# Kernel tuning notes

Measured on AMD Instinct MI355X. Metric: run time of the kernel, lower is better.

The kernel has to match this reference:

```python
import jax, jax.numpy as jnp
import numpy as np

N_NODES = 50000
N_EDGES = 800000
IN_FEATS = 96
HIDDEN = 48


def setup_inputs() -> dict:
    key = jax.random.key(0)
    ks = jax.random.split(key, 16)
    x = jax.random.normal(ks[0], (N_NODES, IN_FEATS), dtype=jnp.float32)
    edge_index = jax.random.randint(ks[1], (2, N_EDGES), 0, N_NODES, dtype=jnp.int32)

    def lin(k, fan_in, fan_out):
        s = 1.0 / np.sqrt(fan_in)
        return jax.random.uniform(k, (fan_in, fan_out), jnp.float32, -s, s)

    return {
        "x": x,
        "edge_index": edge_index,
        # SAGEConv layer 0: in -> hidden
        "w_self0": lin(ks[2], IN_FEATS, HIDDEN),
        "w_neigh0": lin(ks[3], IN_FEATS, HIDDEN),
        "b0": jnp.zeros((HIDDEN,), jnp.float32),
        # SAGEConv layer 1: hidden -> hidden
        "w_self1": lin(ks[4], HIDDEN, HIDDEN),
        "w_neigh1": lin(ks[5], HIDDEN, HIDDEN),
        "b1": jnp.zeros((HIDDEN,), jnp.float32),
        # SAGEConv layer 2: hidden -> hidden
        "w_self2": lin(ks[6], HIDDEN, HIDDEN),
        "w_neigh2": lin(ks[7], HIDDEN, HIDDEN),
        "b2": jnp.zeros((HIDDEN,), jnp.float32),
        # prediction head: hidden -> 1
        "w_pred": lin(ks[8], HIDDEN, 1),
        "b_pred": jnp.zeros((1,), jnp.float32),
    }


def _sage_mean(x, src, dst, deg_inv, w_self, w_neigh, b):
    # mean over in-neighbors: gather src features, segment-sum at dst, / in-degree
    agg = jax.ops.segment_sum(x[src], dst, num_segments=N_NODES) * deg_inv  # [N, F]
    return x @ w_self + agg @ w_neigh + b


def reference(x, edge_index, w_self0, w_neigh0, b0, w_self1, w_neigh1, b1,
              w_self2, w_neigh2, b2, w_pred, b_pred):
    src, dst = edge_index[0], edge_index[1]
    deg = jax.ops.segment_sum(jnp.ones((src.shape[0],), x.dtype), dst,
                              num_segments=N_NODES)
    deg_inv = (1.0 / jnp.maximum(deg, 1.0))[:, None]  # isolated nodes -> 0 agg

    h = jax.nn.relu(_sage_mean(x, src, dst, deg_inv, w_self0, w_neigh0, b0))
    h = jax.nn.relu(_sage_mean(h, src, dst, deg_inv, w_self1, w_neigh1, b1))
    h = jax.nn.relu(_sage_mean(h, src, dst, deg_inv, w_self2, w_neigh2, b2))
    return h @ w_pred + b_pred  # [N, 1]
```

## Files before the change

### kernel.cpp

```cpp
#include <hip/hip_runtime.h>


constexpr int HID = 48;
constexpr int MAXDEG = 64;
constexpr int GNB = 64;

__global__ __launch_bounds__(128) void fill_proj_k(
    const float* __restrict__ X, const float* __restrict__ Wn,
    const float* __restrict__ Ws, const float* __restrict__ bias,
    float* __restrict__ p_out, float* __restrict__ s_out, int n_nodes,
    const int* __restrict__ src, const int* __restrict__ dst,
    int* __restrict__ cnt, unsigned short* __restrict__ buckets,
    int n_edges, int gemm_blocks) {
    __shared__ float wn_lds[96 * HID];
    __shared__ float ws_lds[96 * HID];
    __shared__ float bias_lds[HID];
    const int t = threadIdx.x;

    if ((int)blockIdx.x >= gemm_blocks) {
        int base = (blockIdx.x - gemm_blocks) * 256 + t;
        int e0 = base, e1 = base + 128;
        if (e0 < n_edges) {
            int d = dst[e0];
            int s = src[e0];
            int pos = atomicAdd(&cnt[d], 1);
            if (pos < MAXDEG) buckets[(size_t)d * MAXDEG + pos] = (unsigned short)s;
        }
        if (e1 < n_edges) {
            int d = dst[e1];
            int s = src[e1];
            int pos = atomicAdd(&cnt[d], 1);
            if (pos < MAXDEG) buckets[(size_t)d * MAXDEG + pos] = (unsigned short)s;
        }
        return;
    }

    for (int i = t; i < 96 * HID; i += 128) {
        wn_lds[i] = Wn[i];
        ws_lds[i] = Ws[i];
    }
    if (t < HID) bias_lds[t] = bias[t];
    __syncthreads();

    const int q = t & 3;
    const int m = t >> 2;
    const int jb = q * 12;
    const int n0 = blockIdx.x * GNB + 2 * m;
    const int n1 = n0 + 1;
    const bool v0 = n0 < n_nodes, v1 = n1 < n_nodes;
    const int cn0 = v0 ? n0 : 0, cn1 = v1 ? n1 : 0;

    float pa[12], pb[12], sa[12], sb[12];
#pragma unroll
    for (int j = 0; j < 12; ++j) {
        pa[j] = 0.0f; pb[j] = 0.0f;
        float b = bias_lds[jb + j];
        sa[j] = b; sb[j] = b;
    }

    const float4* xr0 = reinterpret_cast<const float4*>(X + (size_t)cn0 * 96);
    const float4* xr1 = reinterpret_cast<const float4*>(X + (size_t)cn1 * 96);
#pragma unroll 4
    for (int k4 = 0; k4 < 24; ++k4) {
        float4 xa = xr0[k4];
        float4 xb = xr1[k4];
#pragma unroll
        for (int c = 0; c < 4; ++c) {
            float x0 = (c == 0) ? xa.x : (c == 1) ? xa.y : (c == 2) ? xa.z : xa.w;
            float x1 = (c == 0) ? xb.x : (c == 1) ? xb.y : (c == 2) ? xb.z : xb.w;
            const float4* wnr =
                reinterpret_cast<const float4*>(&wn_lds[(k4 * 4 + c) * HID + jb]);
            const float4* wsr =
                reinterpret_cast<const float4*>(&ws_lds[(k4 * 4 + c) * HID + jb]);
#pragma unroll
            for (int j4 = 0; j4 < 3; ++j4) {
                float4 wv = wnr[j4];
                pa[j4 * 4 + 0] = fmaf(x0, wv.x, pa[j4 * 4 + 0]);
                pa[j4 * 4 + 1] = fmaf(x0, wv.y, pa[j4 * 4 + 1]);
                pa[j4 * 4 + 2] = fmaf(x0, wv.z, pa[j4 * 4 + 2]);
                pa[j4 * 4 + 3] = fmaf(x0, wv.w, pa[j4 * 4 + 3]);
                pb[j4 * 4 + 0] = fmaf(x1, wv.x, pb[j4 * 4 + 0]);
                pb[j4 * 4 + 1] = fmaf(x1, wv.y, pb[j4 * 4 + 1]);
                pb[j4 * 4 + 2] = fmaf(x1, wv.z, pb[j4 * 4 + 2]);
                pb[j4 * 4 + 3] = fmaf(x1, wv.w, pb[j4 * 4 + 3]);
                float4 uv = wsr[j4];
                sa[j4 * 4 + 0] = fmaf(x0, uv.x, sa[j4 * 4 + 0]);
                sa[j4 * 4 + 1] = fmaf(x0, uv.y, sa[j4 * 4 + 1]);
                sa[j4 * 4 + 2] = fmaf(x0, uv.z, sa[j4 * 4 + 2]);
                sa[j4 * 4 + 3] = fmaf(x0, uv.w, sa[j4 * 4 + 3]);
                sb[j4 * 4 + 0] = fmaf(x1, uv.x, sb[j4 * 4 + 0]);
                sb[j4 * 4 + 1] = fmaf(x1, uv.y, sb[j4 * 4 + 1]);
                sb[j4 * 4 + 2] = fmaf(x1, uv.z, sb[j4 * 4 + 2]);
                sb[j4 * 4 + 3] = fmaf(x1, uv.w, sb[j4 * 4 + 3]);
            }
        }
    }
    float4* po0 = reinterpret_cast<float4*>(p_out + (size_t)n0 * HID + jb);
    float4* po1 = reinterpret_cast<float4*>(p_out + (size_t)n1 * HID + jb);
    float4* so0 = reinterpret_cast<float4*>(s_out + (size_t)n0 * HID + jb);
    float4* so1 = reinterpret_cast<float4*>(s_out + (size_t)n1 * HID + jb);
#pragma unroll
    for (int j4 = 0; j4 < 3; ++j4) {
        if (v0) {
            po0[j4] = make_float4(pa[j4 * 4 + 0], pa[j4 * 4 + 1], pa[j4 * 4 + 2], pa[j4 * 4 + 3]);
            so0[j4] = make_float4(sa[j4 * 4 + 0], sa[j4 * 4 + 1], sa[j4 * 4 + 2], sa[j4 * 4 + 3]);
        }
        if (v1) {
            po1[j4] = make_float4(pb[j4 * 4 + 0], pb[j4 * 4 + 1], pb[j4 * 4 + 2], pb[j4 * 4 + 3]);
            so1[j4] = make_float4(sb[j4 * 4 + 0], sb[j4 * 4 + 1], sb[j4 * 4 + 2], sb[j4 * 4 + 3]);
        }
    }
}

__device__ __forceinline__ void gather12(const float* __restrict__ p_in,
                                         const unsigned short* __restrict__ bkt,
                                         int deg, int jb, float4 (&g)[3]) {
    float4 ga0 = make_float4(0.f, 0.f, 0.f, 0.f), ga1 = ga0, ga2 = ga0;
    float4 gb0 = ga0, gb1 = ga0, gb2 = ga0;
    int e = 0;
    for (; e + 2 <= deg; e += 2) {
        int s0 = bkt[e], s1 = bkt[e + 1];
        const float4* r0 = reinterpret_cast<const float4*>(p_in + (size_t)s0 * HID + jb);
        const float4* r1 = reinterpret_cast<const float4*>(p_in + (size_t)s1 * HID + jb);
        float4 a0 = r0[0], a1 = r0[1], a2 = r0[2];
        float4 b0 = r1[0], b1 = r1[1], b2 = r1[2];
        ga0.x += a0.x; ga0.y += a0.y; ga0.z += a0.z; ga0.w += a0.w;
        ga1.x += a1.x; ga1.y += a1.y; ga1.z += a1.z; ga1.w += a1.w;
        ga2.x += a2.x; ga2.y += a2.y; ga2.z += a2.z; ga2.w += a2.w;
        gb0.x += b0.x; gb0.y += b0.y; gb0.z += b0.z; gb0.w += b0.w;
        gb1.x += b1.x; gb1.y += b1.y; gb1.z += b1.z; gb1.w += b1.w;
        gb2.x += b2.x; gb2.y += b2.y; gb2.z += b2.z; gb2.w += b2.w;
    }
    if (e < deg) {
        const float4* r0 = reinterpret_cast<const float4*>(p_in + (size_t)bkt[e] * HID + jb);
        float4 a0 = r0[0], a1 = r0[1], a2 = r0[2];
        ga0.x += a0.x; ga0.y += a0.y; ga0.z += a0.z; ga0.w += a0.w;
        ga1.x += a1.x; ga1.y += a1.y; ga1.z += a1.z; ga1.w += a1.w;
        ga2.x += a2.x; ga2.y += a2.y; ga2.z += a2.z; ga2.w += a2.w;
    }
    g[0] = make_float4(ga0.x + gb0.x, ga0.y + gb0.y, ga0.z + gb0.z, ga0.w + gb0.w);
    g[1] = make_float4(ga1.x + gb1.x, ga1.y + gb1.y, ga1.z + gb1.z, ga1.w + gb1.w);
    g[2] = make_float4(ga2.x + gb2.x, ga2.y + gb2.y, ga2.z + gb2.z, ga2.w + gb2.w);
}

template <bool LAST>
__global__ __launch_bounds__(128) void fused_layer_k(
    const float* __restrict__ p_in, const float* __restrict__ s_in,
    const int* __restrict__ cnt, const unsigned short* __restrict__ buckets,
    const float* __restrict__ wn_next, const float* __restrict__ ws_next,
    const float* __restrict__ b_next, const float* __restrict__ w_pred,
    const float* __restrict__ b_pred, float* __restrict__ p_out,
    float* __restrict__ s_out, float* __restrict__ out, int n_nodes) {
    __shared__ float wn_lds[LAST ? 4 : HID * HID];
    __shared__ float ws_lds[LAST ? 4 : HID * HID];
    __shared__ float bn_lds[HID];
    __shared__ float h_tile[LAST ? 4 : GNB * (HID + 1)];
    __shared__ float wpred_lds[HID];

    const int t = threadIdx.x;
    if (!LAST) {
        for (int i = t; i < HID * HID; i += 128) {
            wn_lds[i] = wn_next[i];
            ws_lds[i] = ws_next[i];
        }
        if (t < HID) bn_lds[t] = b_next[t];
    } else {
        if (t < HID) wpred_lds[t] = w_pred[t];
    }
    __syncthreads();

    const int q = t & 3;
    const int m = t >> 2;
    const int jb = q * 12;
    const int n0 = blockIdx.x * GNB + 2 * m;
    const int n1 = n0 + 1;
    const bool v0 = n0 < n_nodes, v1 = n1 < n_nodes;
    const int cn0 = v0 ? n0 : 0, cn1 = v1 ? n1 : 0;

    const int d0 = min(cnt[cn0], MAXDEG);
    const int d1 = min(cnt[cn1], MAXDEG);
    const float di0 = 1.0f / fmaxf((float)d0, 1.0f);
    const float di1 = 1.0f / fmaxf((float)d1, 1.0f);

    float4 g0[3], g1[3];
    gather12(p_in, buckets + (size_t)cn0 * MAXDEG, d0, jb, g0);
    gather12(p_in, buckets + (size_t)cn1 * MAXDEG, d1, jb, g1);

    const float4* sr0 = reinterpret_cast<const float4*>(s_in + (size_t)cn0 * HID + jb);
    const float4* sr1 = reinterpret_cast<const float4*>(s_in + (size_t)cn1 * HID + jb);
    float h0v[12], h1v[12];
#pragma unroll
    for (int j4 = 0; j4 < 3; ++j4) {
        float4 sv0 = sr0[j4];
        float4 sv1 = sr1[j4];
        h0v[j4 * 4 + 0] = fmaxf(fmaf(di0, g0[j4].x, sv0.x), 0.0f);
        h0v[j4 * 4 + 1] = fmaxf(fmaf(di0, g0[j4].y, sv0.y), 0.0f);
        h0v[j4 * 4 + 2] = fmaxf(fmaf(di0, g0[j4].z, sv0.z), 0.0f);
        h0v[j4 * 4 + 3] = fmaxf(fmaf(di0, g0[j4].w, sv0.w), 0.0f);
        h1v[j4 * 4 + 0] = fmaxf(fmaf(di1, g1[j4].x, sv1.x), 0.0f);
        h1v[j4 * 4 + 1] = fmaxf(fmaf(di1, g1[j4].y, sv1.y), 0.0f);
        h1v[j4 * 4 + 2] = fmaxf(fmaf(di1, g1[j4].z, sv1.z), 0.0f);
        h1v[j4 * 4 + 3] = fmaxf(fmaf(di1, g1[j4].w, sv1.w), 0.0f);
    }

    if (LAST) {
        float s0 = 0.0f, s1 = 0.0f;
#pragma unroll
        for (int j = 0; j < 12; ++j) {
            float wp = wpred_lds[jb + j];
            s0 = fmaf(h0v[j], wp, s0);
            s1 = fmaf(h1v[j], wp, s1);
        }
        s0 += __shfl_xor(s0, 1); s0 += __shfl_xor(s0, 2);
        s1 += __shfl_xor(s1, 1); s1 += __shfl_xor(s1, 2);
        if (q == 0) {
            float bp = b_pred[0];
            if (v0) out[n0] = s0 + bp;
            if (v1) out[n1] = s1 + bp;
        }
        return;
    }

    const int ln0 = 2 * m, ln1 = 2 * m + 1;
#pragma unroll
    for (int j = 0; j < 12; ++j) {
        h_tile[ln0 * (HID + 1) + jb + j] = h0v[j];
        h_tile[ln1 * (HID + 1) + jb + j] = h1v[j];
    }
    __syncthreads();

    float pa[12], pb[12], sa[12], sb[12];
#pragma unroll
    for (int j = 0; j < 12; ++j) {
        pa[j] = 0.0f; pb[j] = 0.0f;
        float b = bn_lds[jb + j];
        sa[j] = b; sb[j] = b;
    }
#pragma unroll 4
    for (int k = 0; k < HID; ++k) {
        float ha = h_tile[ln0 * (HID + 1) + k];
        float hb = h_tile[ln1 * (HID + 1) + k];
        const float4* wnr = reinterpret_cast<const float4*>(&wn_lds[k * HID + jb]);
        const float4* wsr = reinterpret_cast<const float4*>(&ws_lds[k * HID + jb]);
#pragma unroll
        for (int j4 = 0; j4 < 3; ++j4) {
            float4 wv = wnr[j4];
            pa[j4 * 4 + 0] = fmaf(ha, wv.x, pa[j4 * 4 + 0]);
            pa[j4 * 4 + 1] = fmaf(ha, wv.y, pa[j4 * 4 + 1]);
            pa[j4 * 4 + 2] = fmaf(ha, wv.z, pa[j4 * 4 + 2]);
            pa[j4 * 4 + 3] = fmaf(ha, wv.w, pa[j4 * 4 + 3]);
            pb[j4 * 4 + 0] = fmaf(hb, wv.x, pb[j4 * 4 + 0]);
            pb[j4 * 4 + 1] = fmaf(hb, wv.y, pb[j4 * 4 + 1]);
            pb[j4 * 4 + 2] = fmaf(hb, wv.z, pb[j4 * 4 + 2]);
            pb[j4 * 4 + 3] = fmaf(hb, wv.w, pb[j4 * 4 + 3]);
            float4 uv = wsr[j4];
            sa[j4 * 4 + 0] = fmaf(ha, uv.x, sa[j4 * 4 + 0]);
            sa[j4 * 4 + 1] = fmaf(ha, uv.y, sa[j4 * 4 + 1]);
            sa[j4 * 4 + 2] = fmaf(ha, uv.z, sa[j4 * 4 + 2]);
            sa[j4 * 4 + 3] = fmaf(ha, uv.w, sa[j4 * 4 + 3]);
            sb[j4 * 4 + 0] = fmaf(hb, uv.x, sb[j4 * 4 + 0]);
            sb[j4 * 4 + 1] = fmaf(hb, uv.y, sb[j4 * 4 + 1]);
            sb[j4 * 4 + 2] = fmaf(hb, uv.z, sb[j4 * 4 + 2]);
            sb[j4 * 4 + 3] = fmaf(hb, uv.w, sb[j4 * 4 + 3]);
        }
    }
    float4* po0 = reinterpret_cast<float4*>(p_out + (size_t)n0 * HID + jb);
    float4* po1 = reinterpret_cast<float4*>(p_out + (size_t)n1 * HID + jb);
    float4* so0 = reinterpret_cast<float4*>(s_out + (size_t)n0 * HID + jb);
    float4* so1 = reinterpret_cast<float4*>(s_out + (size_t)n1 * HID + jb);
#pragma unroll
    for (int j4 = 0; j4 < 3; ++j4) {
        if (v0) {
            po0[j4] = make_float4(pa[j4 * 4 + 0], pa[j4 * 4 + 1], pa[j4 * 4 + 2], pa[j4 * 4 + 3]);
            so0[j4] = make_float4(sa[j4 * 4 + 0], sa[j4 * 4 + 1], sa[j4 * 4 + 2], sa[j4 * 4 + 3]);
        }
        if (v1) {
            po1[j4] = make_float4(pb[j4 * 4 + 0], pb[j4 * 4 + 1], pb[j4 * 4 + 2], pb[j4 * 4 + 3]);
            so1[j4] = make_float4(sb[j4 * 4 + 0], sb[j4 * 4 + 1], sb[j4 * 4 + 2], sb[j4 * 4 + 3]);
        }
    }
}

extern "C" void kernel_launch(void* const* d_in, const int* in_sizes, int n_in,
                              void* d_out, int out_size, void* d_ws, size_t ws_size,
                              hipStream_t stream) {
    const float* x        = (const float*)d_in[0];
    const int*   ei       = (const int*)d_in[1];
    const float* w_self0  = (const float*)d_in[2];
    const float* w_neigh0 = (const float*)d_in[3];
    const float* b0       = (const float*)d_in[4];
    const float* w_self1  = (const float*)d_in[5];
    const float* w_neigh1 = (const float*)d_in[6];
    const float* b1       = (const float*)d_in[7];
    const float* w_self2  = (const float*)d_in[8];
    const float* w_neigh2 = (const float*)d_in[9];
    const float* b2       = (const float*)d_in[10];
    const float* w_pred   = (const float*)d_in[11];
    const float* b_pred   = (const float*)d_in[12];

    const int n_nodes = in_sizes[0] / 96;
    const int n_edges = in_sizes[1] / 2;
    const int* src = ei;
    const int* dst = ei + n_edges;

    char* wsb = (char*)d_ws;
    int* cnt                = (int*)wsb;              wsb += (size_t)n_nodes * 4;
    unsigned short* buckets = (unsigned short*)wsb;   wsb += (size_t)n_nodes * MAXDEG * 2;
    float* pA = (float*)wsb;                          wsb += (size_t)n_nodes * HID * 4;
    float* sA = (float*)wsb;                          wsb += (size_t)n_nodes * HID * 4;
    float* pB = (float*)wsb;                          wsb += (size_t)n_nodes * HID * 4;
    float* sB = (float*)wsb;                          wsb += (size_t)n_nodes * HID * 4;
    float* out = (float*)d_out;

    const int gnb = (n_nodes + GNB - 1) / GNB;
    const int fb = (n_edges + 255) / 256;

    hipMemsetAsync(cnt, 0, (size_t)n_nodes * 4, stream);

    fill_proj_k<<<gnb + fb, 128, 0, stream>>>(x, w_neigh0, w_self0, b0, pA, sA,
                                              n_nodes, src, dst, cnt, buckets,
                                              n_edges, gnb);
    fused_layer_k<false><<<gnb, 128, 0, stream>>>(pA, sA, cnt, buckets,
                                                  w_neigh1, w_self1, b1,
                                                  nullptr, nullptr, pB, sB,
                                                  nullptr, n_nodes);
    fused_layer_k<false><<<gnb, 128, 0, stream>>>(pB, sB, cnt, buckets,
                                                  w_neigh2, w_self2, b2,
                                                  nullptr, nullptr, pA, sA,
                                                  nullptr, n_nodes);
    fused_layer_k<true><<<gnb, 128, 0, stream>>>(pA, sA, cnt, buckets,
                                                 nullptr, nullptr, nullptr,
                                                 w_pred, b_pred, nullptr,
                                                 nullptr, out, n_nodes);
}
```

Before: 244.4 us.

## Split per-node gather across lanes and halve LDS in first projection

The fused layer kernel now gives each node 8 lanes instead of 4, with lane pairs gathering alternate neighbors and combining sums through wavefront shuffles. The next-layer projection is split over K between the two halves using shuffles instead of an LDS h tile, and blocks cover 16 nodes with launch bounds hinting 4 blocks per CU. The first kernel reuses one LDS weight buffer for both projections in two passes, which halves its LDS footprint but reads X twice and adds barriers. The aim is more parallelism and latency hiding for the random gathers, at the cost of extra shuffle traffic and 4x as many blocks.

```diff
diff --git a/kernel.cpp b/kernel.cpp
--- a/kernel.cpp
+++ b/kernel.cpp
@@ -12,8 +12,7 @@
     const int* __restrict__ src, const int* __restrict__ dst,
     int* __restrict__ cnt, unsigned short* __restrict__ buckets,
     int n_edges, int gemm_blocks) {
-    __shared__ float wn_lds[96 * HID];
-    __shared__ float ws_lds[96 * HID];
+    __shared__ float wlds[96 * HID];
     __shared__ float bias_lds[HID];
     const int t = threadIdx.x;
 
@@ -35,13 +34,6 @@
         return;
     }
 
-    for (int i = t; i < 96 * HID; i += 128) {
-        wn_lds[i] = Wn[i];
-        ws_lds[i] = Ws[i];
-    }
-    if (t < HID) bias_lds[t] = bias[t];
-    __syncthreads();
-
     const int q = t & 3;
     const int m = t >> 2;
     const int jb = q * 12;
@@ -49,102 +41,99 @@
     const int n1 = n0 + 1;
     const bool v0 = n0 < n_nodes, v1 = n1 < n_nodes;
     const int cn0 = v0 ? n0 : 0, cn1 = v1 ? n1 : 0;
-
-    float pa[12], pb[12], sa[12], sb[12];
-#pragma unroll
-    for (int j = 0; j < 12; ++j) {
-        pa[j] = 0.0f; pb[j] = 0.0f;
-        float b = bias_lds[jb + j];
-        sa[j] = b; sb[j] = b;
-    }
-
     const float4* xr0 = reinterpret_cast<const float4*>(X + (size_t)cn0 * 96);
     const float4* xr1 = reinterpret_cast<const float4*>(X + (size_t)cn1 * 96);
+
+    for (int i = t; i < 96 * HID; i += 128) wlds[i] = Wn[i];
+    __syncthreads();
+    {
+        float pa[12], pb[12];
+#pragma unroll
+        for (int j = 0; j < 12; ++j) { pa[j] = 0.0f; pb[j] = 0.0f; }
 #pragma unroll 4
-    for (int k4 = 0; k4 < 24; ++k4) {
-        float4 xa = xr0[k4];
-        float4 xb = xr1[k4];
-#pragma unroll
-        for (int c = 0; c < 4; ++c) {
-            float x0 = (c == 0) ? xa.x : (c == 1) ? xa.y : (c == 2) ? xa.z : xa.w;
-            float x1 = (c == 0) ? xb.x : (c == 1) ? xb.y : (c == 2) ? xb.z : xb.w;
-            const float4* wnr =
-                reinterpret_cast<const float4*>(&wn_lds[(k4 * 4 + c) * HID + jb]);
-            const float4* wsr =
-                reinterpret_cast<const float4*>(&ws_lds[(k4 * 4 + c) * HID + jb]);
-#pragma unroll
-            for (int j4 = 0; j4 < 3; ++j4) {
-                float4 wv = wnr[j4];
-                pa[j4 * 4 + 0] = fmaf(x0, wv.x, pa[j4 * 4 + 0]);
-                pa[j4 * 4 + 1] = fmaf(x0, wv.y, pa[j4 * 4 + 1]);
-                pa[j4 * 4 + 2] = fmaf(x0, wv.z, pa[j4 * 4 + 2]);
-                pa[j4 * 4 + 3] = fmaf(x0, wv.w, pa[j4 * 4 + 3]);
-                pb[j4 * 4 + 0] = fmaf(x1, wv.x, pb[j4 * 4 + 0]);
-                pb[j4 * 4 + 1] = fmaf(x1, wv.y, pb[j4 * 4 + 1]);
-                pb[j4 * 4 + 2] = fmaf(x1, wv.z, pb[j4 * 4 + 2]);
-                pb[j4 * 4 + 3] = fmaf(x1, wv.w, pb[j4 * 4 + 3]);
-                float4 uv = wsr[j4];
-                sa[j4 * 4 + 0] = fmaf(x0, uv.x, sa[j4 * 4 + 0]);
-                sa[j4 * 4 + 1] = fmaf(x0, uv.y, sa[j4 * 4 + 1]);
-                sa[j4 * 4 + 2] = fmaf(x0, uv.z, sa[j4 * 4 + 2]);
-                sa[j4 * 4 + 3] = fmaf(x0, uv.w, sa[j4 * 4 + 3]);
-                sb[j4 * 4 + 0] = fmaf(x1, uv.x, sb[j4 * 4 + 0]);
-                sb[j4 * 4 + 1] = fmaf(x1, uv.y, sb[j4 * 4 + 1]);
-                sb[j4 * 4 + 2] = fmaf(x1, uv.z, sb[j4 * 4 + 2]);
-                sb[j4 * 4 + 3] = fmaf(x1, uv.w, sb[j4 * 4 + 3]);
+        for (int k4 = 0; k4 < 24; ++k4) {
+            float4 xa = xr0[k4];
+            float4 xb = xr1[k4];
+#pragma unroll
+            for (int c = 0; c < 4; ++c) {
+                float x0 = (c == 0) ? xa.x : (c == 1) ? xa.y : (c == 2) ? xa.z : xa.w;
+                float x1 = (c == 0) ? xb.x : (c == 1) ? xb.y : (c == 2) ? xb.z : xb.w;
+                const float4* wr =
+                    reinterpret_cast<const float4*>(&wlds[(k4 * 4 + c) * HID + jb]);
+#pragma unroll
+                for (int j4 = 0; j4 < 3; ++j4) {
+                    float4 wv = wr[j4];
+                    pa[j4 * 4 + 0] = fmaf(x0, wv.x, pa[j4 * 4 + 0]);
+                    pa[j4 * 4 + 1] = fmaf(x0, wv.y, pa[j4 * 4 + 1]);
+                    pa[j4 * 4 + 2] = fmaf(x0, wv.z, pa[j4 * 4 + 2]);
+                    pa[j4 * 4 + 3] = fmaf(x0, wv.w, pa[j4 * 4 + 3]);
+                    pb[j4 * 4 + 0] = fmaf(x1, wv.x, pb[j4 * 4 + 0]);
+                    pb[j4 * 4 + 1] = fmaf(x1, wv.y, pb[j4 * 4 + 1]);
+                    pb[j4 * 4 + 2] = fmaf(x1, wv.z, pb[j4 * 4 + 2]);
+                    pb[j4 * 4 + 3] = fmaf(x1, wv.w, pb[j4 * 4 + 3]);
+                }
             }
         }
-    }
-    float4* po0 = reinterpret_cast<float4*>(p_out + (size_t)n0 * HID + jb);
-    float4* po1 = reinterpret_cast<float4*>(p_out + (size_t)n1 * HID + jb);
-    float4* so0 = reinterpret_cast<float4*>(s_out + (size_t)n0 * HID + jb);
-    float4* so1 = reinterpret_cast<float4*>(s_out + (size_t)n1 * HID + jb);
-#pragma unroll
-    for (int j4 = 0; j4 < 3; ++j4) {
-        if (v0) {
-            po0[j4] = make_float4(pa[j4 * 4 + 0], pa[j4 * 4 + 1], pa[j4 * 4 + 2], pa[j4 * 4 + 3]);
-            so0[j4] = make_float4(sa[j4 * 4 + 0], sa[j4 * 4 + 1], sa[j4 * 4 + 2], sa[j4 * 4 + 3]);
-        }
-        if (v1) {
-            po1[j4] = make_float4(pb[j4 * 4 + 0], pb[j4 * 4 + 1], pb[j4 * 4 + 2], pb[j4 * 4 + 3]);
-            so1[j4] = make_float4(sb[j4 * 4 + 0], sb[j4 * 4 + 1], sb[j4 * 4 + 2], sb[j4 * 4 + 3]);
+        float4* po0 = reinterpret_cast<float4*>(p_out + (size_t)n0 * HID + jb);
+        float4* po1 = reinterpret_cast<float4*>(p_out + (size_t)n1 * HID + jb);
+#pragma unroll
+        for (int j4 = 0; j4 < 3; ++j4) {
+            if (v0) po0[j4] = make_float4(pa[j4 * 4 + 0], pa[j4 * 4 + 1],
+                                          pa[j4 * 4 + 2], pa[j4 * 4 + 3]);
+            if (v1) po1[j4] = make_float4(pb[j4 * 4 + 0], pb[j4 * 4 + 1],
+                                          pb[j4 * 4 + 2], pb[j4 * 4 + 3]);
+        }
+    }
+    __syncthreads();
+
+    for (int i = t; i < 96 * HID; i += 128) wlds[i] = Ws[i];
+    if (t < HID) bias_lds[t] = bias[t];
+    __syncthreads();
+    {
+        float sa[12], sb[12];
+#pragma unroll
+        for (int j = 0; j < 12; ++j) {
+            float b = bias_lds[jb + j];
+            sa[j] = b; sb[j] = b;
+        }
+#pragma unroll 4
+        for (int k4 = 0; k4 < 24; ++k4) {
+            float4 xa = xr0[k4];
+            float4 xb = xr1[k4];
+#pragma unroll
+            for (int c = 0; c < 4; ++c) {
+                float x0 = (c == 0) ? xa.x : (c == 1) ? xa.y : (c == 2) ? xa.z : xa.w;
+                float x1 = (c == 0) ? xb.x : (c == 1) ? xb.y : (c == 2) ? xb.z : xb.w;
+                const float4* wr =
+                    reinterpret_cast<const float4*>(&wlds[(k4 * 4 + c) * HID + jb]);
+#pragma unroll
+                for (int j4 = 0; j4 < 3; ++j4) {
+                    float4 wv = wr[j4];
+                    sa[j4 * 4 + 0] = fmaf(x0, wv.x, sa[j4 * 4 + 0]);
+                    sa[j4 * 4 + 1] = fmaf(x0, wv.y, sa[j4 * 4 + 1]);
+                    sa[j4 * 4 + 2] = fmaf(x0, wv.z, sa[j4 * 4 + 2]);
+                    sa[j4 * 4 + 3] = fmaf(x0, wv.w, sa[j4 * 4 + 3]);
+                    sb[j4 * 4 + 0] = fmaf(x1, wv.x, sb[j4 * 4 + 0]);
+                    sb[j4 * 4 + 1] = fmaf(x1, wv.y, sb[j4 * 4 + 1]);
+                    sb[j4 * 4 + 2] = fmaf(x1, wv.z, sb[j4 * 4 + 2]);
+                    sb[j4 * 4 + 3] = fmaf(x1, wv.w, sb[j4 * 4 + 3]);
+                }
+            }
+        }
+        float4* so0 = reinterpret_cast<float4*>(s_out + (size_t)n0 * HID + jb);
+        float4* so1 = reinterpret_cast<float4*>(s_out + (size_t)n1 * HID + jb);
+#pragma unroll
+        for (int j4 = 0; j4 < 3; ++j4) {
+            if (v0) so0[j4] = make_float4(sa[j4 * 4 + 0], sa[j4 * 4 + 1],
+                                          sa[j4 * 4 + 2], sa[j4 * 4 + 3]);
+            if (v1) so1[j4] = make_float4(sb[j4 * 4 + 0], sb[j4 * 4 + 1],
+                                          sb[j4 * 4 + 2], sb[j4 * 4 + 3]);
         }
     }
 }
 
-__device__ __forceinline__ void gather12(const float* __restrict__ p_in,
-                                         const unsigned short* __restrict__ bkt,
-                                         int deg, int jb, float4 (&g)[3]) {
-    float4 ga0 = make_float4(0.f, 0.f, 0.f, 0.f), ga1 = ga0, ga2 = ga0;
-    float4 gb0 = ga0, gb1 = ga0, gb2 = ga0;
-    int e = 0;
-    for (; e + 2 <= deg; e += 2) {
-        int s0 = bkt[e], s1 = bkt[e + 1];
-        const float4* r0 = reinterpret_cast<const float4*>(p_in + (size_t)s0 * HID + jb);
-        const float4* r1 = reinterpret_cast<const float4*>(p_in + (size_t)s1 * HID + jb);
-        float4 a0 = r0[0], a1 = r0[1], a2 = r0[2];
-        float4 b0 = r1[0], b1 = r1[1], b2 = r1[2];
-        ga0.x += a0.x; ga0.y += a0.y; ga0.z += a0.z; ga0.w += a0.w;
-        ga1.x += a1.x; ga1.y += a1.y; ga1.z += a1.z; ga1.w += a1.w;
-        ga2.x += a2.x; ga2.y += a2.y; ga2.z += a2.z; ga2.w += a2.w;
-        gb0.x += b0.x; gb0.y += b0.y; gb0.z += b0.z; gb0.w += b0.w;
-        gb1.x += b1.x; gb1.y += b1.y; gb1.z += b1.z; gb1.w += b1.w;
-        gb2.x += b2.x; gb2.y += b2.y; gb2.z += b2.z; gb2.w += b2.w;
-    }
-    if (e < deg) {
-        const float4* r0 = reinterpret_cast<const float4*>(p_in + (size_t)bkt[e] * HID + jb);
-        float4 a0 = r0[0], a1 = r0[1], a2 = r0[2];
-        ga0.x += a0.x; ga0.y += a0.y; ga0.z += a0.z; ga0.w += a0.w;
-        ga1.x += a1.x; ga1.y += a1.y; ga1.z += a1.z; ga1.w += a1.w;
-        ga2.x += a2.x; ga2.y += a2.y; ga2.z += a2.z; ga2.w += a2.w;
-    }
-    g[0] = make_float4(ga0.x + gb0.x, ga0.y + gb0.y, ga0.z + gb0.z, ga0.w + gb0.w);
-    g[1] = make_float4(ga1.x + gb1.x, ga1.y + gb1.y, ga1.z + gb1.z, ga1.w + gb1.w);
-    g[2] = make_float4(ga2.x + gb2.x, ga2.y + gb2.y, ga2.z + gb2.z, ga2.w + gb2.w);
-}
-
 template <bool LAST>
-__global__ __launch_bounds__(128) void fused_layer_k(
+__global__ __launch_bounds__(128, 4) void fused_layer_k(
     const float* __restrict__ p_in, const float* __restrict__ s_in,
     const int* __restrict__ cnt, const unsigned short* __restrict__ buckets,
     const float* __restrict__ wn_next, const float* __restrict__ ws_next,
@@ -154,8 +143,7 @@
     __shared__ float wn_lds[LAST ? 4 : HID * HID];
     __shared__ float ws_lds[LAST ? 4 : HID * HID];
     __shared__ float bn_lds[HID];
-    __shared__ float h_tile[LAST ? 4 : GNB * (HID + 1)];
-    __shared__ float wpred_lds[HID];
+    __shared__ float wp_lds[HID];
 
     const int t = threadIdx.x;
     if (!LAST) {
@@ -165,119 +153,125 @@
         }
         if (t < HID) bn_lds[t] = b_next[t];
     } else {
-        if (t < HID) wpred_lds[t] = w_pred[t];
+        if (t < HID) wp_lds[t] = w_pred[t];
     }
     __syncthreads();
 
     const int q = t & 3;
-    const int m = t >> 2;
+    const int e = (t >> 2) & 1;
+    const int m = t >> 3;
+    const int n = blockIdx.x * 16 + m;
+    if (n >= n_nodes) return;
     const int jb = q * 12;
-    const int n0 = blockIdx.x * GNB + 2 * m;
-    const int n1 = n0 + 1;
-    const bool v0 = n0 < n_nodes, v1 = n1 < n_nodes;
-    const int cn0 = v0 ? n0 : 0, cn1 = v1 ? n1 : 0;
-
-    const int d0 = min(cnt[cn0], MAXDEG);
-    const int d1 = min(cnt[cn1], MAXDEG);
-    const float di0 = 1.0f / fmaxf((float)d0, 1.0f);
-    const float di1 = 1.0f / fmaxf((float)d1, 1.0f);
-
-    float4 g0[3], g1[3];
-    gather12(p_in, buckets + (size_t)cn0 * MAXDEG, d0, jb, g0);
-    gather12(p_in, buckets + (size_t)cn1 * MAXDEG, d1, jb, g1);
-
-    const float4* sr0 = reinterpret_cast<const float4*>(s_in + (size_t)cn0 * HID + jb);
-    const float4* sr1 = reinterpret_cast<const float4*>(s_in + (size_t)cn1 * HID + jb);
-    float h0v[12], h1v[12];
+
+    const int deg = min(cnt[n], MAXDEG);
+    const float di = 1.0f / fmaxf((float)deg, 1.0f);
+    const unsigned short* bkt = buckets + (size_t)n * MAXDEG;
+
+    float4 ga[3], gb[3];
+#pragma unroll
+    for (int c = 0; c < 3; ++c) {
+        ga[c] = make_float4(0.f, 0.f, 0.f, 0.f);
+        gb[c] = make_float4(0.f, 0.f, 0.f, 0.f);
+    }
+    int i = e;
+    for (; i + 2 < deg; i += 4) {
+        int s0 = bkt[i], s1 = bkt[i + 2];
+        const float4* r0 = reinterpret_cast<const float4*>(p_in + (size_t)s0 * HID + jb);
+        const float4* r1 = reinterpret_cast<const float4*>(p_in + (size_t)s1 * HID + jb);
+#pragma unroll
+        for (int c = 0; c < 3; ++c) {
+            float4 a = r0[c], b = r1[c];
+            ga[c].x += a.x; ga[c].y += a.y; ga[c].z += a.z; ga[c].w += a.w;
+            gb[c].x += b.x; gb[c].y += b.y; gb[c].z += b.z; gb[c].w += b.w;
+        }
+    }
+    if (i < deg) {
+        int s0 = bkt[i];
+        const float4* r0 = reinterpret_cast<const float4*>(p_in + (size_t)s0 * HID + jb);
+#pragma unroll
+        for (int c = 0; c < 3; ++c) {
+            float4 a = r0[c];
+            ga[c].x += a.x; ga[c].y += a.y; ga[c].z += a.z; ga[c].w += a.w;
+        }
+    }
+    float g[12];
+#pragma unroll
+    for (int c = 0; c < 3; ++c) {
+        g[c * 4 + 0] = ga[c].x + gb[c].x;
+        g[c * 4 + 1] = ga[c].y + gb[c].y;
+        g[c * 4 + 2] = ga[c].z + gb[c].z;
+        g[c * 4 + 3] = ga[c].w + gb[c].w;
+    }
+#pragma unroll
+    for (int j = 0; j < 12; ++j) g[j] += __shfl_xor(g[j], 4, 64);
+
+    const float4* sr = reinterpret_cast<const float4*>(s_in + (size_t)n * HID + jb);
+    float h[12];
 #pragma unroll
     for (int j4 = 0; j4 < 3; ++j4) {
-        float4 sv0 = sr0[j4];
-        float4 sv1 = sr1[j4];
-        h0v[j4 * 4 + 0] = fmaxf(fmaf(di0, g0[j4].x, sv0.x), 0.0f);
-        h0v[j4 * 4 + 1] = fmaxf(fmaf(di0, g0[j4].y, sv0.y), 0.0f);
-        h0v[j4 * 4 + 2] = fmaxf(fmaf(di0, g0[j4].z, sv0.z), 0.0f);
-        h0v[j4 * 4 + 3] = fmaxf(fmaf(di0, g0[j4].w, sv0.w), 0.0f);
-        h1v[j4 * 4 + 0] = fmaxf(fmaf(di1, g1[j4].x, sv1.x), 0.0f);
-        h1v[j4 * 4 + 1] = fmaxf(fmaf(di1, g1[j4].y, sv1.y), 0.0f);
-        h1v[j4 * 4 + 2] = fmaxf(fmaf(di1, g1[j4].z, sv1.z), 0.0f);
-        h1v[j4 * 4 + 3] = fmaxf(fmaf(di1, g1[j4].w, sv1.w), 0.0f);
+        float4 sv = sr[j4];
+        h[j4 * 4 + 0] = fmaxf(fmaf(di, g[j4 * 4 + 0], sv.x), 0.0f);
+        h[j4 * 4 + 1] = fmaxf(fmaf(di, g[j4 * 4 + 1], sv.y), 0.0f);
+        h[j4 * 4 + 2] = fmaxf(fmaf(di, g[j4 * 4 + 2], sv.z), 0.0f);
+        h[j4 * 4 + 3] = fmaxf(fmaf(di, g[j4 * 4 + 3], sv.w), 0.0f);
     }
 
     if (LAST) {
-        float s0 = 0.0f, s1 = 0.0f;
-#pragma unroll
-        for (int j = 0; j < 12; ++j) {
-            float wp = wpred_lds[jb + j];
-            s0 = fmaf(h0v[j], wp, s0);
-            s1 = fmaf(h1v[j], wp, s1);
-        }
-        s0 += __shfl_xor(s0, 1); s0 += __shfl_xor(s0, 2);
-        s1 += __shfl_xor(s1, 1); s1 += __shfl_xor(s1, 2);
-        if (q == 0) {
-            float bp = b_pred[0];
-            if (v0) out[n0] = s0 + bp;
-            if (v1) out[n1] = s1 + bp;
-        }
+        float s = 0.0f;
+#pragma unroll
+        for (int j = 0; j < 12; ++j) s = fmaf(h[j], wp_lds[jb + j], s);
+        s += __shfl_xor(s, 1, 64);
+        s += __shfl_xor(s, 2, 64);
+        if ((t & 7) == 0) out[n] = s + b_pred[0];
         return;
     }
 
-    const int ln0 = 2 * m, ln1 = 2 * m + 1;
+    float pa[12], sa[12];
 #pragma unroll
     for (int j = 0; j < 12; ++j) {
-        h_tile[ln0 * (HID + 1) + jb + j] = h0v[j];
-        h_tile[ln1 * (HID + 1) + jb + j] = h1v[j];
-    }
-    __syncthreads();
-
-    float pa[12], pb[12], sa[12], sb[12];
-#pragma unroll
-    for (int j = 0; j < 12; ++j) {
-        pa[j] = 0.0f; pb[j] = 0.0f;
-        float b = bn_lds[jb + j];
-        sa[j] = b; sb[j] = b;
-    }
-#pragma unroll 4
-    for (int k = 0; k < HID; ++k) {
-        float ha = h_tile[ln0 * (HID + 1) + k];
-        float hb = h_tile[ln1 * (HID + 1) + k];
+        pa[j] = 0.0f;
+        sa[j] = (e == 0) ? bn_lds[jb + j] : 0.0f;
+    }
+    const int kb = e * 24;
+#pragma unroll
+    for (int kk = 0; kk < 24; ++kk) {
+        const int k = kb + kk;
+        const int srcl = (t & ~3) | (k / 12);
+        float hs = __shfl(h[kk % 12], srcl, 64);
         const float4* wnr = reinterpret_cast<const float4*>(&wn_lds[k * HID + jb]);
         const float4* wsr = reinterpret_cast<const float4*>(&ws_lds[k * HID + jb]);
 #pragma unroll
         for (int j4 = 0; j4 < 3; ++j4) {
             float4 wv = wnr[j4];
-            pa[j4 * 4 + 0] = fmaf(ha, wv.x, pa[j4 * 4 + 0]);
-            pa[j4 * 4 + 1] = fmaf(ha, wv.y, pa[j4 * 4 + 1]);
-            pa[j4 * 4 + 2] = fmaf(ha, wv.z, pa[j4 * 4 + 2]);
-            pa[j4 * 4 + 3] = fmaf(ha, wv.w, pa[j4 * 4 + 3]);
-            pb[j4 * 4 + 0] = fmaf(hb, wv.x, pb[j4 * 4 + 0]);
-            pb[j4 * 4 + 1] = fmaf(hb, wv.y, pb[j4 * 4 + 1]);
-            pb[j4 * 4 + 2] = fmaf(hb, wv.z, pb[j4 * 4 + 2]);
-            pb[j4 * 4 + 3] = fmaf(hb, wv.w, pb[j4 * 4 + 3]);
+            pa[j4 * 4 + 0] = fmaf(hs, wv.x, pa[j4 * 4 + 0]);
+            pa[j4 * 4 + 1] = fmaf(hs, wv.y, pa[j4 * 4 + 1]);
+            pa[j4 * 4 + 2] = fmaf(hs, wv.z, pa[j4 * 4 + 2]);
+            pa[j4 * 4 + 3] = fmaf(hs, wv.w, pa[j4 * 4 + 3]);
             float4 uv = wsr[j4];
-            sa[j4 * 4 + 0] = fmaf(ha, uv.x, sa[j4 * 4 + 0]);
-            sa[j4 * 4 + 1] = fmaf(ha, uv.y, sa[j4 * 4 + 1]);
-            sa[j4 * 4 + 2] = fmaf(ha, uv.z, sa[j4 * 4 + 2]);
-            sa[j4 * 4 + 3] = fmaf(ha, uv.w, sa[j4 * 4 + 3]);
-            sb[j4 * 4 + 0] = fmaf(hb, uv.x, sb[j4 * 4 + 0]);
-            sb[j4 * 4 + 1] = fmaf(hb, uv.y, sb[j4 * 4 + 1]);
-            sb[j4 * 4 + 2] = fmaf(hb, uv.z, sb[j4 * 4 + 2]);
-            sb[j4 * 4 + 3] = fmaf(hb, uv.w, sb[j4 * 4 + 3]);
-        }
-    }
-    float4* po0 = reinterpret_cast<float4*>(p_out + (size_t)n0 * HID + jb);
-    float4* po1 = reinterpret_cast<float4*>(p_out + (size_t)n1 * HID + jb);
-    float4* so0 = reinterpret_cast<float4*>(s_out + (size_t)n0 * HID + jb);
-    float4* so1 = reinterpret_cast<float4*>(s_out + (size_t)n1 * HID + jb);
-#pragma unroll
-    for (int j4 = 0; j4 < 3; ++j4) {
-        if (v0) {
-            po0[j4] = make_float4(pa[j4 * 4 + 0], pa[j4 * 4 + 1], pa[j4 * 4 + 2], pa[j4 * 4 + 3]);
-            so0[j4] = make_float4(sa[j4 * 4 + 0], sa[j4 * 4 + 1], sa[j4 * 4 + 2], sa[j4 * 4 + 3]);
-        }
-        if (v1) {
-            po1[j4] = make_float4(pb[j4 * 4 + 0], pb[j4 * 4 + 1], pb[j4 * 4 + 2], pb[j4 * 4 + 3]);
-            so1[j4] = make_float4(sb[j4 * 4 + 0], sb[j4 * 4 + 1], sb[j4 * 4 + 2], sb[j4 * 4 + 3]);
-        }
+            sa[j4 * 4 + 0] = fmaf(hs, uv.x, sa[j4 * 4 + 0]);
+            sa[j4 * 4 + 1] = fmaf(hs, uv.y, sa[j4 * 4 + 1]);
+            sa[j4 * 4 + 2] = fmaf(hs, uv.z, sa[j4 * 4 + 2]);
+            sa[j4 * 4 + 3] = fmaf(hs, uv.w, sa[j4 * 4 + 3]);
+        }
+    }
+#pragma unroll
+    for (int j = 0; j < 12; ++j) {
+        pa[j] += __shfl_xor(pa[j], 4, 64);
+        sa[j] += __shfl_xor(sa[j], 4, 64);
+    }
+    if (e == 0) {
+        float4* po = reinterpret_cast<float4*>(p_out + (size_t)n * HID + jb);
+#pragma unroll
+        for (int j4 = 0; j4 < 3; ++j4)
+            po[j4] = make_float4(pa[j4 * 4 + 0], pa[j4 * 4 + 1],
+                                 pa[j4 * 4 + 2], pa[j4 * 4 + 3]);
+    } else {
+        float4* so = reinterpret_cast<float4*>(s_out + (size_t)n * HID + jb);
+#pragma unroll
+        for (int j4 = 0; j4 < 3; ++j4)
+            so[j4] = make_float4(sa[j4 * 4 + 0], sa[j4 * 4 + 1],
+                                 sa[j4 * 4 + 2], sa[j4 * 4 + 3]);
     }
 }
 
@@ -314,22 +308,23 @@
 
     const int gnb = (n_nodes + GNB - 1) / GNB;
     const int fb = (n_edges + 255) / 256;
+    const int lb = (n_nodes + 15) / 16;
 
     hipMemsetAsync(cnt, 0, (size_t)n_nodes * 4, stream);
 
     fill_proj_k<<<gnb + fb, 128, 0, stream>>>(x, w_neigh0, w_self0, b0, pA, sA,
                                               n_nodes, src, dst, cnt, buckets,
                                               n_edges, gnb);
-    fused_layer_k<false><<<gnb, 128, 0, stream>>>(pA, sA, cnt, buckets,
-                                                  w_neigh1, w_self1, b1,
-                                                  nullptr, nullptr, pB, sB,
-                                                  nullptr, n_nodes);
-    fused_layer_k<false><<<gnb, 128, 0, stream>>>(pB, sB, cnt, buckets,
-                                                  w_neigh2, w_self2, b2,
-                                                  nullptr, nullptr, pA, sA,
-                                                  nullptr, n_nodes);
-    fused_layer_k<true><<<gnb, 128, 0, stream>>>(pA, sA, cnt, buckets,
-                                                 nullptr, nullptr, nullptr,
-                                                 w_pred, b_pred, nullptr,
-                                                 nullptr, out, n_nodes);
+    fused_layer_k<false><<<lb, 128, 0, stream>>>(pA, sA, cnt, buckets,
+                                                 w_neigh1, w_self1, b1,
+                                                 nullptr, nullptr, pB, sB,
+                                                 nullptr, n_nodes);
+    fused_layer_k<false><<<lb, 128, 0, stream>>>(pB, sB, cnt, buckets,
+                                                 w_neigh2, w_self2, b2,
+                                                 nullptr, nullptr, pA, sA,
+                                                 nullptr, n_nodes);
+    fused_layer_k<true><<<lb, 128, 0, stream>>>(pA, sA, cnt, buckets,
+                                                nullptr, nullptr, nullptr,
+                                                w_pred, b_pred, nullptr,
+                                                nullptr, out, n_nodes);
 }
```

Result: no change. 246.8 us (+1.0%).
